# Kernel optimization log

Hardware: AMD Instinct MI355X
Metric: run time of the kernel (lower is better)

## Reference

```python
import jax, jax.numpy as jnp
import numpy as np

B, C, H, W = 128, 512, 14, 14
WIN, SHIFT = 7, 3
HEADS, HD = 16, 32
HID = 2048
EPS = 1e-5
N = WIN * WIN
NWH = H // WIN
NW = NWH * NWH


def _rel_pos_index():
    coords = np.stack(np.meshgrid(np.arange(WIN), np.arange(WIN), indexing='ij'))  # (2,Wh,Ww)
    flat = coords.reshape(2, -1)
    rel = (flat[:, :, None] - flat[:, None, :]).transpose(1, 2, 0)  # (N,N,2)
    rel[..., 0] += WIN - 1
    rel[..., 1] += WIN - 1
    rel[..., 0] *= 2 * WIN - 1
    return rel.sum(-1)  # (N,N) in [0, (2W-1)^2)


def _attn_mask():
    img = np.zeros((H, W))
    cnt = 0
    for h in (slice(0, -WIN), slice(-WIN, -SHIFT), slice(-SHIFT, None)):
        for w in (slice(0, -WIN), slice(-WIN, -SHIFT), slice(-SHIFT, None)):
            img[h, w] = cnt
            cnt += 1
    mw = img.reshape(NWH, WIN, NWH, WIN).transpose(0, 2, 1, 3).reshape(-1, N)  # (nW,N)
    d = mw[:, None, :] - mw[:, :, None]
    return np.where(d != 0, -100.0, 0.0).astype(np.float32)  # (nW,N,N)


REL_IDX = _rel_pos_index()
ATTN_MASK = jnp.asarray(_attn_mask())


def _ln_c(x, w, b):
    # LayerNorm2d: normalize over channel dim of NCHW
    mu = x.mean(axis=1, keepdims=True)
    var = ((x - mu) ** 2).mean(axis=1, keepdims=True)
    xn = (x - mu) * jax.lax.rsqrt(var + EPS)
    return xn * w[None, :, None, None] + b[None, :, None, None]


def setup_inputs() -> dict:
    key = jax.random.key(0)
    ks = jax.random.split(key, 12)
    s = 0.02
    return {
        'x': jax.random.normal(ks[0], (B, C, H, W), jnp.float32),
        'ln1_w': jnp.ones((C,), jnp.float32),
        'ln1_b': jnp.zeros((C,), jnp.float32),
        'qkv_w': jax.random.normal(ks[1], (3 * C, C), jnp.float32) * s,
        'qkv_b': jnp.zeros((3 * C,), jnp.float32),
        'rel_bias': jax.random.normal(ks[2], ((2 * WIN - 1) ** 2, HEADS), jnp.float32) * s,
        'proj_w': jax.random.normal(ks[3], (C, C), jnp.float32) * s,
        'proj_b': jnp.zeros((C,), jnp.float32),
        'gamma1': jnp.full((C,), 1e-6, jnp.float32),
        'ln2_w': jnp.ones((C,), jnp.float32),
        'ln2_b': jnp.zeros((C,), jnp.float32),
        'fc1_w': jax.random.normal(ks[4], (HID, C), jnp.float32) * s,
        'fc1_b': jnp.zeros((HID,), jnp.float32),
        'fc2_w': jax.random.normal(ks[5], (C, HID), jnp.float32) * s,
        'fc2_b': jnp.zeros((C,), jnp.float32),
        'gamma2': jnp.full((C,), 1e-6, jnp.float32),
    }


def reference(x, ln1_w, ln1_b, qkv_w, qkv_b, rel_bias, proj_w, proj_b, gamma1,
              ln2_w, ln2_b, fc1_w, fc1_b, fc2_w, fc2_b, gamma2):
    # ---- shifted-window attention branch ----
    y = _ln_c(x, ln1_w, ln1_b).transpose(0, 2, 3, 1)  # (B,H,W,C)
    y = jnp.roll(y, (-SHIFT, -SHIFT), axis=(1, 2))
    # window partition -> (B*nW, N, C)
    xw = y.reshape(B, NWH, WIN, NWH, WIN, C).transpose(0, 1, 3, 2, 4, 5).reshape(B * NW, N, C)
    qkv = (xw @ qkv_w.T + qkv_b).reshape(B * NW, N, 3, HEADS, HD).transpose(2, 0, 3, 1, 4)
    q, k, v = qkv[0], qkv[1], qkv[2]  # (B*nW, heads, N, hd)
    attn = jnp.einsum('bhnd,bhmd->bhnm', q * (HD ** -0.5), k)
    bias = rel_bias[REL_IDX.reshape(-1)].reshape(N, N, HEADS).transpose(2, 0, 1)  # (heads,N,N)
    attn = attn + bias[None]
    attn = attn.reshape(B, NW, HEADS, N, N) + ATTN_MASK[None, :, None]
    attn = jax.nn.softmax(attn.reshape(B * NW, HEADS, N, N), axis=-1)
    out = jnp.einsum('bhnm,bhmd->bhnd', attn, v).transpose(0, 2, 1, 3).reshape(B * NW, N, C)
    out = out @ proj_w.T + proj_b
    # window reverse + roll back
    y = out.reshape(B, NWH, NWH, WIN, WIN, C).transpose(0, 1, 3, 2, 4, 5).reshape(B, H, W, C)
    y = jnp.roll(y, (SHIFT, SHIFT), axis=(1, 2))
    y = gamma1 * y  # layer scale over channel (last dim in NHWC)
    x = x + y.transpose(0, 3, 1, 2)
    # ---- MLP branch ----
    z = _ln_c(x, ln2_w, ln2_b).transpose(0, 2, 3, 1)  # (B,H,W,C)
    z = jax.nn.gelu(z @ fc1_w.T + fc1_b, approximate=False)
    z = z @ fc2_w.T + fc2_b
    z = gamma2 * z
    return x + z.transpose(0, 3, 1, 2)
```

## Files before the change

### kernel.cpp

```cpp
#include <hip/hip_runtime.h>
#include <cmath>
#include <cstdint>

typedef float floatx4 __attribute__((ext_vector_type(4)));
typedef float floatx16 __attribute__((ext_vector_type(16)));
typedef int   intx4   __attribute__((ext_vector_type(4)));
typedef int   intx8   __attribute__((ext_vector_type(8)));

#define EPS_ 1e-5f
#define QSCALE 0.17677669529663689f

__device__ __forceinline__ void gload16(const uint8_t* g, uint8_t* l) {
  __builtin_amdgcn_global_load_lds(
      (const __attribute__((address_space(1))) void*)g,
      (__attribute__((address_space(3))) void*)l, 16, 0, 0);
}

template<bool HI>
__device__ __forceinline__ int pk_fp8(float a, float b, int old) {
  return __builtin_amdgcn_cvt_pk_fp8_f32(a, b, old, HI);
}
__device__ __forceinline__ int pk_fp8x4(float v0, float v1, float v2, float v3) {
  int w = pk_fp8<false>(v0, v1, 0);
  return pk_fp8<true>(v2, v3, w);
}

__device__ __forceinline__ uint16_t f2bf(float f) {
  uint32_t u = __float_as_uint(f);
  return (uint16_t)((u + 0x7fffu + ((u >> 16) & 1u)) >> 16);
}
__device__ __forceinline__ float bf2f(uint16_t h) {
  return __uint_as_float(((uint32_t)h) << 16);
}

__device__ __forceinline__ float fast_gelu(float v) {
  const float t = __expf(-1.702f * v);
  return v * __builtin_amdgcn_rcpf(1.f + t);
}

__device__ __forceinline__ intx8 cat8(intx4 a, intx4 b) {
  return __builtin_shufflevector(a, b, 0, 1, 2, 3, 4, 5, 6, 7);
}
__device__ __forceinline__ floatx16 mfma_mx(intx8 a, intx8 b, floatx16 c) {
  return __builtin_amdgcn_mfma_scale_f32_32x32x64_f8f6f4(
      a, b, c, 0, 0, 0, 0x7F7F7F7F, 0, 0x7F7F7F7F);
}


template<int K>
__global__ void cvt_frag(const float* __restrict__ s, uint8_t* __restrict__ d, int n4) {
  const int i = blockIdx.x * 256 + threadIdx.x;
  if (i >= n4) return;
  const int kq = K >> 2;
  const int n = i / kq;
  const int k = (i - n * kq) << 2;
  const float4 v = ((const float4*)s)[i];
  const int panel = ((n >> 6) << 2) + (n & 3);
  const int lm = (n >> 2) & 15;
  const long addr = (long)panel * (16 * K) + ((k >> 3) << 7) + (lm << 3) + (k & 4);
  *(int*)(d + addr) = pk_fp8x4(v.x, v.y, v.z, v.w);
}

__global__ void cvt_frag_mx512(const float* __restrict__ s, uint8_t* __restrict__ d, int n4) {
  const int i = blockIdx.x * 256 + threadIdx.x;
  if (i >= n4) return;
  const int n = i >> 7;
  const int k = (i & 127) << 2;
  const float4 v = ((const float4*)s)[i];
  const long addr = (long)(n >> 6) * 32768 + (n & 1) * 16384 + ((k >> 6) << 11)
                  + (((k >> 4) & 1) << 10)
                  + ((((k >> 5) & 1) << 5) + ((n & 63) >> 1)) * 16 + (k & 15);
  *(int*)(d + addr) = pk_fp8x4(v.x, v.y, v.z, v.w);
}

__global__ __launch_bounds__(256)
void ln_stats_nchw(const float* __restrict__ x, float* __restrict__ mu, float* __restrict__ rs) {
  const int tl = threadIdx.x & 63;
  const int wv = threadIdx.x >> 6;
  const int t = blockIdx.x * 64 + tl;
  const int b = t / 196;
  const int p = t - b * 196;
  const float* xp = x + (long)b * 100352 + p;
  float s = 0.f, ss = 0.f;
  const int cbeg = wv * 128;
  for (int c = cbeg; c < cbeg + 128; ++c) {
    const float v = xp[(long)c * 196];
    s += v; ss += v * v;
  }
  __shared__ float sb[4][64], qb[4][64];
  sb[wv][tl] = s; qb[wv][tl] = ss;
  __syncthreads();
  if (wv == 0) {
    s  = sb[0][tl] + sb[1][tl] + sb[2][tl] + sb[3][tl];
    ss = qb[0][tl] + qb[1][tl] + qb[2][tl] + qb[3][tl];
    const float m = s * (1.f / 512.f);
    const float var = ss * (1.f / 512.f) - m * m;
    mu[t] = m;
    rs[t] = rsqrtf(var + EPS_);
  }
}

__global__ __launch_bounds__(256)
void ln1_apply(const float* __restrict__ x, const float* __restrict__ mu, const float* __restrict__ rs,
               const float* __restrict__ w, const float* __restrict__ bb, uint8_t* __restrict__ A) {
  __shared__ float tile[64][53];
  const int bid = blockIdx.x;
  const int ct = bid & 7;
  const int pt = (bid >> 3) & 3;
  const int b = bid >> 5;
  const int p0 = pt * 49, c0 = ct * 64;
  const long xbase = (long)b * 100352;
  for (int idx = threadIdx.x; idx < 3136; idx += 256) {
    const int cl = idx / 49;
    const int pl = idx - cl * 49;
    tile[cl][pl] = x[xbase + (long)(c0 + cl) * 196 + p0 + pl];
  }
  __syncthreads();
  const int tbase = b * 196 + p0;
  for (int idx = threadIdx.x; idx < 784; idx += 256) {
    const int pl = idx >> 4;
    const int cq = (idx & 15) << 2;
    const int t = tbase + pl;
    const int c = c0 + cq;
    const float m = mu[t], rr = rs[t];
    const float v0 = (tile[cq + 0][pl] - m) * rr * w[c + 0] + bb[c + 0];
    const float v1 = (tile[cq + 1][pl] - m) * rr * w[c + 1] + bb[c + 1];
    const float v2 = (tile[cq + 2][pl] - m) * rr * w[c + 2] + bb[c + 2];
    const float v3 = (tile[cq + 3][pl] - m) * rr * w[c + 3] + bb[c + 3];
    const long addr = (long)(t & ~15) * 512 + ((c >> 3) << 7) + ((t & 15) << 3) + (c & 4);
    *(int*)(A + addr) = pk_fp8x4(v0, v1, v2, v3);
  }
}

__global__ __launch_bounds__(256)
void ln2_panel(const uint16_t* __restrict__ Xb, const float* __restrict__ S1,
               const float* __restrict__ S2, const float* __restrict__ w,
               const float* __restrict__ bb, uint8_t* __restrict__ Z) {
  __shared__ float xs[16 * 516];
  const int p = blockIdx.x;
  const int t0 = p * 16;
  for (int idx = threadIdx.x; idx < 1024; idx += 256) {
    const int tl = idx >> 6;
    const int c8 = (idx & 63) << 3;
    const uint4 raw = *(const uint4*)(Xb + ((long)(t0 + tl) << 9) + c8);
    float* xr = xs + tl * 516 + c8;
    xr[0] = bf2f((uint16_t)(raw.x & 0xffff)); xr[1] = bf2f((uint16_t)(raw.x >> 16));
    xr[2] = bf2f((uint16_t)(raw.y & 0xffff)); xr[3] = bf2f((uint16_t)(raw.y >> 16));
    xr[4] = bf2f((uint16_t)(raw.z & 0xffff)); xr[5] = bf2f((uint16_t)(raw.z >> 16));
    xr[6] = bf2f((uint16_t)(raw.w & 0xffff)); xr[7] = bf2f((uint16_t)(raw.w >> 16));
  }
  __syncthreads();
  for (int e = threadIdx.x; e < 2048; e += 256) {
    const int tl = e >> 7;
    const int c  = (e & 127) << 2;
    const int t = t0 + tl;
    const float m = S1[t] * (1.f / 512.f);
    const float var = S2[t] * (1.f / 512.f) - m * m;
    const float r = rsqrtf(var + EPS_);
    const float* xr = xs + tl * 516 + c;
    const float v0 = (xr[0] - m) * r * w[c + 0] + bb[c + 0];
    const float v1 = (xr[1] - m) * r * w[c + 1] + bb[c + 1];
    const float v2 = (xr[2] - m) * r * w[c + 2] + bb[c + 2];
    const float v3 = (xr[3] - m) * r * w[c + 3] + bb[c + 3];
    const long addr = (long)(t >> 5) * 16384 + ((c >> 5) << 10) + ((t & 31) << 5) + (c & 31);
    *(int*)(Z + addr) = pk_fp8x4(v0, v1, v2, v3);
  }
}

template<int MI, int K, int EPI, int NG, int T>
__global__ __launch_bounds__(256, 4)
void gemm_bl(const uint8_t* __restrict__ A, const uint8_t* __restrict__ Bw,
             const float* __restrict__ bias, const float* __restrict__ res,
             const uint16_t* __restrict__ resb, const float* __restrict__ gamma,
             uint8_t* __restrict__ outb, float* __restrict__ outf,
             uint16_t* __restrict__ outh, float* __restrict__ S1, float* __restrict__ S2,
             const int N) {
  const int kx = blockIdx.x & 7;
  const int sx = blockIdx.x >> 3;
  const int t = (sx / NG) * 8 + kx;
  if (t >= T) return;
  const int g = sx - (sx / NG) * NG;
  __shared__ __align__(16) uint8_t Bs[(EPI == 3) ? 33280 : 32768];
  const int tid = threadIdx.x;
  const int wave = tid >> 6, lane = tid & 63;
  const int lm = lane & 15, lq = lane >> 4;
  const long m0 = (long)t * (MI * 64);
  const long n0 = (long)g << 6;
  const uint8_t* abase = A + (m0 + wave * MI * 16) * (long)K + (lane << 3);
  floatx4 acc[MI][4] = {};
  constexpr int NKS = K / 32;
  long aP0[MI], aP1[MI];
  #pragma unroll
  for (int i = 0; i < MI; ++i) {
    aP0[i] = *(const long*)(abase + (long)i * 16 * K);
    aP1[i] = *(const long*)(abase + (long)i * 16 * K + 512);
  }
  #pragma unroll
  for (int ph = 0; ph < K / 512; ++ph) {
    const uint8_t* bsrc = Bw + n0 * K + ph * 8192;
    #pragma unroll
    for (int j = 0; j < 4; ++j)
      #pragma unroll
      for (int c = 0; c < 2; ++c)
        gload16(bsrc + (long)j * 16 * K + c * 4096 + tid * 16,
                Bs + j * 8192 + c * 4096 + tid * 16);
    __syncthreads();
    #pragma unroll
    for (int ksl = 0; ksl < 16; ++ksl) {
      const int sg = ph * 16 + ksl;
      long aC[MI];
      #pragma unroll
      for (int i = 0; i < MI; ++i) aC[i] = (ksl & 1) ? aP1[i] : aP0[i];
      if (sg + 2 < NKS) {
        #pragma unroll
        for (int i = 0; i < MI; ++i) {
          const long v = *(const long*)(abase + (long)i * 16 * K + (long)(sg + 2) * 512);
          if (ksl & 1) aP1[i] = v; else aP0[i] = v;
        }
      }
      long bf[4];
      #pragma unroll
      for (int j = 0; j < 4; ++j)
        bf[j] = *(const long*)(Bs + j * 8192 + ksl * 512 + (lane << 3));
      __builtin_amdgcn_s_setprio(1);
      #pragma unroll
      for (int i = 0; i < MI; ++i)
        #pragma unroll
        for (int j = 0; j < 4; ++j)
          acc[i][j] = __builtin_amdgcn_mfma_f32_16x16x32_fp8_fp8(aC[i], bf[j], acc[i][j], 0, 0, 0);
      __builtin_amdgcn_s_setprio(0);
    }
    if (K / 512 > 1 && ph + 1 < K / 512) __syncthreads();
  }
  const int cb = (g << 6) + (lm << 2);
  const float4 b4 = *(const float4*)(bias + cb);
  float4 g4 = make_float4(0.f, 0.f, 0.f, 0.f);
  if (EPI == 1 || EPI == 3) g4 = *(const float4*)(gamma + cb);
  const float qs = (EPI == 0 && cb < 512) ? QSCALE : 1.f;
  if (EPI != 3) {
    #pragma unroll
    for (int i = 0; i < MI; ++i) {
      #pragma unroll
      for (int r = 0; r < 4; ++r) {
        const long rowg = m0 + wave * MI * 16 + i * 16 + lq * 4 + r;
        float v0 = acc[i][0][r] + b4.x;
        float v1 = acc[i][1][r] + b4.y;
        float v2 = acc[i][2][r] + b4.z;
        float v3 = acc[i][3][r] + b4.w;
        if (EPI == 0) {
          *(int*)(outb + rowg * (long)N + cb) = pk_fp8x4(v0 * qs, v1 * qs, v2 * qs, v3 * qs);
        } else {
          const unsigned rg = (unsigned)rowg;
          const unsigned bi = rg / 196u;
          const unsigned p = rg - bi * 196u;
          const float* xr = res + (long)bi * 100352 + p;
          const float o0 = xr[(long)(cb + 0) * 196] + g4.x * v0;
          const float o1 = xr[(long)(cb + 1) * 196] + g4.y * v1;
          const float o2 = xr[(long)(cb + 2) * 196] + g4.z * v2;
          const float o3 = xr[(long)(cb + 3) * 196] + g4.w * v3;
          ushort4 hv;
          hv.x = f2bf(o0); hv.y = f2bf(o1); hv.z = f2bf(o2); hv.w = f2bf(o3);
          *(ushort4*)(outh + rowg * 512 + cb) = hv;
          const float q0 = bf2f(hv.x), q1 = bf2f(hv.y), q2 = bf2f(hv.z), q3 = bf2f(hv.w);
          float s = q0 + q1 + q2 + q3;
          float ss = q0 * q0 + q1 * q1 + q2 * q2 + q3 * q3;
          s += __shfl_xor(s, 1);  ss += __shfl_xor(ss, 1);
          s += __shfl_xor(s, 2);  ss += __shfl_xor(ss, 2);
          s += __shfl_xor(s, 4);  ss += __shfl_xor(ss, 4);
          s += __shfl_xor(s, 8);  ss += __shfl_xor(ss, 8);
          if (lm == 0) {
            atomicAdd(S1 + rowg, s);
            atomicAdd(S2 + rowg, ss);
          }
        }
      }
    }
  } else {
    float* Tx = (float*)Bs;
    __syncthreads();
    #pragma unroll
    for (int i = 0; i < MI; ++i) {
      #pragma unroll
      for (int r = 0; r < 4; ++r) {
        const long rowg = m0 + wave * MI * 16 + i * 16 + lq * 4 + r;
        const int rl = (int)(rowg - m0);
        const ushort4 rb = *(const ushort4*)(resb + rowg * 512 + cb);
        Tx[(lm * 4 + 0) * 129 + rl] = bf2f(rb.x) + g4.x * (acc[i][0][r] + b4.x);
        Tx[(lm * 4 + 1) * 129 + rl] = bf2f(rb.y) + g4.y * (acc[i][1][r] + b4.y);
        Tx[(lm * 4 + 2) * 129 + rl] = bf2f(rb.z) + g4.z * (acc[i][2][r] + b4.z);
        Tx[(lm * 4 + 3) * 129 + rl] = bf2f(rb.w) + g4.w * (acc[i][3][r] + b4.w);
      }
    }
    __syncthreads();
    #pragma unroll
    for (int t2 = 0; t2 < 32; ++t2) {
      const int idx = t2 * 256 + tid;
      const int rl = idx & 127;
      const int ch = idx >> 7;
      const unsigned m = (unsigned)(m0 + rl);
      const unsigned bi = m / 196u;
      const unsigned p = m - bi * 196u;
      outf[(long)bi * 100352 + (long)(n0 + ch) * 196 + p] = Tx[ch * 129 + rl];
    }
  }
}

__global__ __launch_bounds__(256, 4)
void gemm_mx_fc1(const uint8_t* __restrict__ A, const uint8_t* __restrict__ Bw,
                 const float* __restrict__ bias, uint8_t* __restrict__ outb) {
  const int kx = blockIdx.x & 7;
  const int sx = blockIdx.x >> 3;
  const int t = (sx >> 5) * 8 + kx;
  if (t >= 98) return;
  const int g = sx & 31;
  __shared__ __align__(16) uint8_t Bs[32768];
  const int tid = threadIdx.x;
  const int wave = tid >> 6, lane = tid & 63;
  const long m0 = (long)t * 256;
  const int n0 = g << 6;
  const uint8_t* bsrc = Bw + (long)n0 * 512;
  #pragma unroll
  for (int c = 0; c < 8; ++c)
    gload16(bsrc + c * 4096 + tid * 16, Bs + c * 4096 + tid * 16);
  const uint8_t* ab0 = A + (m0 + wave * 64) * 512 + lane * 32;
  const uint8_t* ab1 = ab0 + 16384;
  floatx16 acc[2][2] = {};
  __syncthreads();
  #pragma unroll
  for (int s = 0; s < 8; ++s) {
    const intx8 a0 = cat8(*(const intx4*)(ab0 + s * 2048), *(const intx4*)(ab0 + s * 2048 + 16));
    const intx8 a1 = cat8(*(const intx4*)(ab1 + s * 2048), *(const intx4*)(ab1 + s * 2048 + 16));
    const intx8 b0 = cat8(*(const intx4*)(Bs + s * 2048 + lane * 16),
                          *(const intx4*)(Bs + s * 2048 + 1024 + lane * 16));
    const intx8 b1 = cat8(*(const intx4*)(Bs + 16384 + s * 2048 + lane * 16),
                          *(const intx4*)(Bs + 16384 + s * 2048 + 1024 + lane * 16));
    acc[0][0] = mfma_mx(a0, b0, acc[0][0]);
    acc[0][1] = mfma_mx(a0, b1, acc[0][1]);
    acc[1][0] = mfma_mx(a1, b0, acc[1][0]);
    acc[1][1] = mfma_mx(a1, b1, acc[1][1]);
  }
  __syncthreads();
  uint8_t* Ex = Bs;
  const int cp = lane & 31;
  const int hl = cp << 1;
  const float2 b2 = *(const float2*)(bias + n0 + hl);
  const int hoff = ((hl >> 3) << 4) + (hl & 7);
  #pragma unroll
  for (int ri = 0; ri < 2; ++ri)
    #pragma unroll
    for (int q = 0; q < 16; ++q) {
      const int ml = wave * 64 + ri * 32 + 4 * (lane >> 5) + (q & 3) + 8 * (q >> 2);
      const float v0 = fast_gelu(acc[ri][0][q] + b2.x);
      const float v1 = fast_gelu(acc[ri][1][q] + b2.y);
      const int w = pk_fp8<false>(v0, v1, 0);
      const int laddr = ((ml >> 4) << 10) + (((ml & 15) >> 1) << 7) + ((ml & 1) << 3) + hoff;
      *(uint16_t*)(Ex + laddr) = (uint16_t)(w & 0xffff);
    }
  __syncthreads();
  #pragma unroll
  for (int t2 = 0; t2 < 4; ++t2) {
    const int u = t2 * 256 + tid;
    const long gaddr = (m0 + ((u >> 6) << 4)) * 2048 + (((long)(n0 >> 3) + (u & 7)) << 7)
                     + (((u >> 3) & 7) << 4);
    *(int4*)(outb + gaddr) = *(const int4*)(Ex + u * 16);
  }
}

__global__ __launch_bounds__(256)
void bm_build(const float* __restrict__ rel_bias, float* __restrict__ BM) {
  const int hw = blockIdx.x;
  const int head = hw >> 2, wpos = hw & 3;
  const int wi = wpos >> 1, wj = wpos & 1;
  for (int k = 0; k < 4; ++k) {
    const int idx = k * 256 + threadIdx.x;
    const int tile = idx >> 6, l = idx & 63;
    const int qi = tile >> 2, ti = tile & 3;
    const int n = l & 15, g = l >> 4;
    const int query = qi * 16 + n;
    const int qy = query / 7, qx = query - qy * 7;
    const int hh = wi * 7 + qy, ww = wj * 7 + qx;
    const int ri = (hh < 7 ? 0 : (hh < 11 ? 1 : 2)) * 3 + (ww < 7 ? 0 : (ww < 11 ? 1 : 2));
    float4 ov;
    float vv[4];
    #pragma unroll
    for (int r = 0; r < 4; ++r) {
      const int key = ti * 16 + g * 4 + r;
      float v;
      if (query >= 49 || key >= 49) {
        v = -3.0e38f;
      } else {
        const int ky = key / 7, kx = key - ky * 7;
        const int bidx = (qy - ky + 6) * 13 + (qx - kx + 6);
        const int h2 = wi * 7 + ky, w2 = wj * 7 + kx;
        const int rj = (h2 < 7 ? 0 : (h2 < 11 ? 1 : 2)) * 3 + (w2 < 7 ? 0 : (w2 < 11 ? 1 : 2));
        v = rel_bias[bidx * 16 + head] + ((ri != rj) ? -100.f : 0.f);
      }
      vv[r] = v;
    }
    ov.x = vv[0]; ov.y = vv[1]; ov.z = vv[2]; ov.w = vv[3];
    *(float4*)(BM + ((long)(hw * 16 + tile) << 8) + l * 4) = ov;
  }
}

__device__ __forceinline__ void tr4(const uint32_t d[4], uint32_t o[4]) {
  #pragma unroll
  for (int c = 0; c < 4; ++c)
    o[c] = ((d[0] >> (8 * c)) & 0xffu) | (((d[1] >> (8 * c)) & 0xffu) << 8)
         | (((d[2] >> (8 * c)) & 0xffu) << 16) | (((d[3] >> (8 * c)) & 0xffu) << 24);
}

__global__ __launch_bounds__(256)
void attn_mfma(const uint8_t* __restrict__ QKV, const float* __restrict__ BM,
               uint8_t* __restrict__ AT) {
  __shared__ uint8_t lds[4][9984];
  const int wave = threadIdx.x >> 6, lane = threadIdx.x & 63;
  const int n = lane & 15, g = lane >> 4;
  const int gw = blockIdx.x * 4 + wave;
  const int wd = gw >> 4, head = gw & 15;
  const int b = wd >> 2, wpos = wd & 3;
  const int wi = wpos >> 1, wj = wpos & 1;
  uint8_t* Pb = lds[wave];
  uint8_t* Vt = lds[wave] + 4608;
  uint8_t* Ot = lds[wave] + 6912;
  const long base = (long)b * 196 * 1536;
  auto tok = [&](int slot) -> int {
    const int ty = slot / 7, tx = slot - ty * 7;
    int h = wi * 7 + ty + 3; if (h >= 14) h -= 14;
    int w = wj * 7 + tx + 3; if (w >= 14) w -= 14;
    return h * 14 + w;
  };
  long Ak[4], Bq[4];
  #pragma unroll
  for (int t4 = 0; t4 < 4; ++t4) {
    int slot = t4 * 16 + n; if (slot > 48) slot = 48;
    const long tb = base + (long)tok(slot) * 1536 + head * 32 + g * 8;
    Bq[t4] = *(const long*)(QKV + tb);
    Ak[t4] = *(const long*)(QKV + tb + 512);
  }
  #pragma unroll
  for (int bb2 = 0; bb2 < 2; ++bb2) {
    const int blk = lane + bb2 * 64;
    const int dq = blk >> 4, tq = blk & 15;
    uint32_t d4[4], o4[4];
    #pragma unroll
    for (int r = 0; r < 4; ++r) {
      int slot = tq * 4 + r; if (slot > 48) slot = 48;
      d4[r] = *(const uint32_t*)(QKV + base + (long)tok(slot) * 1536 + 1024 + head * 32 + dq * 4);
    }
    tr4(d4, o4);
    #pragma unroll
    for (int c = 0; c < 4; ++c)
      *(uint32_t*)(Vt + (dq * 4 + c) * 72 + tq * 4) = o4[c];
  }
  floatx4 acc[4][4];
  const float* bmw = BM + ((long)(head * 4 + wpos) << 12) + lane * 4;
  #pragma unroll
  for (int qi = 0; qi < 4; ++qi)
    #pragma unroll
    for (int ti = 0; ti < 4; ++ti) {
      const float4 bv = *(const float4*)(bmw + ((qi * 4 + ti) << 8));
      acc[qi][ti][0] = bv.x; acc[qi][ti][1] = bv.y;
      acc[qi][ti][2] = bv.z; acc[qi][ti][3] = bv.w;
    }
  #pragma unroll
  for (int qi = 0; qi < 4; ++qi)
    #pragma unroll
    for (int ti = 0; ti < 4; ++ti)
      acc[qi][ti] = __builtin_amdgcn_mfma_f32_16x16x32_fp8_fp8(Ak[ti], Bq[qi], acc[qi][ti], 0, 0, 0);
  #pragma unroll
  for (int qi = 0; qi < 4; ++qi) {
    float mx = -3.0e38f;
    #pragma unroll
    for (int ti = 0; ti < 4; ++ti)
      #pragma unroll
      for (int r = 0; r < 4; ++r) mx = fmaxf(mx, acc[qi][ti][r]);
    mx = fmaxf(mx, __shfl_xor(mx, 16));
    mx = fmaxf(mx, __shfl_xor(mx, 32));
    float sum = 0.f;
    #pragma unroll
    for (int ti = 0; ti < 4; ++ti)
      #pragma unroll
      for (int r = 0; r < 4; ++r) {
        const float e = __expf(acc[qi][ti][r] - mx);
        acc[qi][ti][r] = e; sum += e;
      }
    sum += __shfl_xor(sum, 16);
    sum += __shfl_xor(sum, 32);
    const float inv = 1.f / sum;
    #pragma unroll
    for (int ti = 0; ti < 4; ++ti) {
      const int pw = pk_fp8x4(acc[qi][ti][0] * inv, acc[qi][ti][1] * inv,
                              acc[qi][ti][2] * inv, acc[qi][ti][3] * inv);
      *(uint32_t*)(Pb + (qi * 16 + n) * 72 + ti * 16 + g * 4) = pw;
    }
  }
  asm volatile("s_waitcnt lgkmcnt(0)" ::: "memory");
  long Bv[2][2];
  #pragma unroll
  for (int ni = 0; ni < 2; ++ni)
    #pragma unroll
    for (int s = 0; s < 2; ++s)
      Bv[ni][s] = *(const long*)(Vt + (ni * 16 + n) * 72 + s * 32 + g * 8);
  floatx4 o[4][2] = {};
  #pragma unroll
  for (int qi = 0; qi < 4; ++qi)
    #pragma unroll
    for (int s = 0; s < 2; ++s) {
      const long Ap = *(const long*)(Pb + (qi * 16 + n) * 72 + s * 32 + g * 8);
      #pragma unroll
      for (int ni = 0; ni < 2; ++ni)
        o[qi][ni] = __builtin_amdgcn_mfma_f32_16x16x32_fp8_fp8(Ap, Bv[ni][s], o[qi][ni], 0, 0, 0);
    }
  #pragma unroll
  for (int qi = 0; qi < 4; ++qi)
    #pragma unroll
    for (int ni = 0; ni < 2; ++ni)
      #pragma unroll
      for (int r = 0; r < 4; ++r)
        Ot[(qi * 16 + g * 4 + r) * 48 + ni * 16 + n] =
            (uint8_t)(pk_fp8<false>(o[qi][ni][r], 0.f, 0) & 0xff);
  asm volatile("s_waitcnt lgkmcnt(0)" ::: "memory");
  if (lane < 49) {
    const int m = b * 196 + tok(lane);
    uint8_t* opb = AT + (long)(m & ~15) * 512 + ((m & 15) << 3);
    #pragma unroll
    for (int d8 = 0; d8 < 4; ++d8)
      *(long*)(opb + (head * 4 + d8) * 128) = *(const long*)(Ot + lane * 48 + d8 * 8);
  }
}

extern "C" void kernel_launch(void* const* d_in, const int* in_sizes, int n_in,
                              void* d_out, int out_size, void* d_ws, size_t ws_size,
                              hipStream_t stream) {
  const float* x      = (const float*)d_in[0];
  const float* ln1_w  = (const float*)d_in[1];
  const float* ln1_b  = (const float*)d_in[2];
  const float* qkv_w  = (const float*)d_in[3];
  const float* qkv_b  = (const float*)d_in[4];
  const float* relb   = (const float*)d_in[5];
  const float* proj_w = (const float*)d_in[6];
  const float* proj_b = (const float*)d_in[7];
  const float* gamma1 = (const float*)d_in[8];
  const float* ln2_w  = (const float*)d_in[9];
  const float* ln2_b  = (const float*)d_in[10];
  const float* fc1_w  = (const float*)d_in[11];
  const float* fc1_b  = (const float*)d_in[12];
  const float* fc2_w  = (const float*)d_in[13];
  const float* fc2_b  = (const float*)d_in[14];
  const float* gamma2 = (const float*)d_in[15];
  float* out = (float*)d_out;
  char* ws = (char*)d_ws;

  float*    mu1 = (float*)(ws + 0);
  float*    rs1 = (float*)(ws + 100352);
  float*    S1  = (float*)(ws + 200704);
  float*    S2  = (float*)(ws + 301056);
  uint8_t*  Wq  = (uint8_t*)(ws + 401408);
  uint8_t*  Wp  = (uint8_t*)(ws + 1187840);
  uint8_t*  W1  = (uint8_t*)(ws + 1449984);
  uint8_t*  W2  = (uint8_t*)(ws + 2498560);
  float*    BMt = (float*)  (ws + 3547136);
  uint8_t*  Afp = (uint8_t*)(ws + 4595712);
  uint16_t* X1b = (uint16_t*)(ws + 68820992);
  uint8_t*  QKV = (uint8_t*)(ws + 120201216);
  uint8_t*  AT  = (uint8_t*)(ws + 158736384);
  uint8_t*  Hb  = (uint8_t*)(ws + 120201216);

  hipMemsetAsync(ws + 200704, 0, 200704, stream);

  cvt_frag<512> <<<768,  256, 0, stream>>>(qkv_w, Wq, 196608);
  cvt_frag<512> <<<256,  256, 0, stream>>>(proj_w, Wp, 65536);
  cvt_frag_mx512<<<1024, 256, 0, stream>>>(fc1_w, W1, 262144);
  cvt_frag<2048><<<1024, 256, 0, stream>>>(fc2_w, W2, 262144);
  bm_build<<<64, 256, 0, stream>>>(relb, BMt);

  ln_stats_nchw<<<392, 256, 0, stream>>>(x, mu1, rs1);
  ln1_apply<<<4096, 256, 0, stream>>>(x, mu1, rs1, ln1_w, ln1_b, Afp);

  gemm_bl<4, 512, 0, 24, 98><<<2496, 256, 0, stream>>>(Afp, Wq, qkv_b, nullptr, nullptr, nullptr, QKV, nullptr, nullptr, nullptr, nullptr, 1536);

  attn_mfma<<<2048, 256, 0, stream>>>(QKV, BMt, AT);

  gemm_bl<4, 512, 1, 8, 98><<<832, 256, 0, stream>>>(AT, Wp, proj_b, x, nullptr, gamma1, nullptr, nullptr, X1b, S1, S2, 512);

  ln2_panel<<<1568, 256, 0, stream>>>(X1b, S1, S2, ln2_w, ln2_b, Afp);

  gemm_mx_fc1<<<3328, 256, 0, stream>>>(Afp, W1, fc1_b, Hb);

  gemm_bl<2, 2048, 3, 8, 196><<<1600, 256, 0, stream>>>(Hb, W2, fc2_b, nullptr, X1b, gamma2, nullptr, out, nullptr, nullptr, nullptr, 512);
}
```

Baseline: 372.6 us.

## Move fc2 GEMM to MX fp8 32x32 MFMA kernel with matching hidden layout

Replaces the fc2 GEMM, which used the generic 16x16x32 fp8 kernel with 128-row tiles, with a dedicated kernel using the scaled 32x32 MX MFMA and 256x64 tiles, as already done for fc1. The fc1 epilogue now writes the hidden activation in the fragment layout this kernel expects, and fc2 weights are converted with a generalized MX fragment converter. The NCHW transpose epilogue runs in two halves through LDS to fit the larger tile. The aim is higher MFMA throughput and fewer, larger blocks. The cost is more output per block and a more serialized two-pass epilogue.

```diff
diff --git a/kernel.cpp b/kernel.cpp
--- a/kernel.cpp
+++ b/kernel.cpp
@@ -61,13 +61,15 @@
   *(int*)(d + addr) = pk_fp8x4(v.x, v.y, v.z, v.w);
 }
 
-__global__ void cvt_frag_mx512(const float* __restrict__ s, uint8_t* __restrict__ d, int n4) {
+template<int K>
+__global__ void cvt_frag_mx(const float* __restrict__ s, uint8_t* __restrict__ d, int n4) {
   const int i = blockIdx.x * 256 + threadIdx.x;
   if (i >= n4) return;
-  const int n = i >> 7;
-  const int k = (i & 127) << 2;
+  const int kq = K >> 2;
+  const int n = i / kq;
+  const int k = (i - n * kq) << 2;
   const float4 v = ((const float4*)s)[i];
-  const long addr = (long)(n >> 6) * 32768 + (n & 1) * 16384 + ((k >> 6) << 11)
+  const long addr = (long)(n >> 6) * (64 * K) + (long)(n & 1) * (32 * K) + ((k >> 6) << 11)
                   + (((k >> 4) & 1) << 10)
                   + ((((k >> 5) & 1) << 5) + ((n & 63) >> 1)) * 16 + (k & 15);
   *(int*)(d + addr) = pk_fp8x4(v.x, v.y, v.z, v.w);
@@ -171,8 +173,8 @@
 __global__ __launch_bounds__(256, 4)
 void gemm_bl(const uint8_t* __restrict__ A, const uint8_t* __restrict__ Bw,
              const float* __restrict__ bias, const float* __restrict__ res,
-             const uint16_t* __restrict__ resb, const float* __restrict__ gamma,
-             uint8_t* __restrict__ outb, float* __restrict__ outf,
+             const float* __restrict__ gamma,
+             uint8_t* __restrict__ outb,
              uint16_t* __restrict__ outh, float* __restrict__ S1, float* __restrict__ S2,
              const int N) {
   const int kx = blockIdx.x & 7;
@@ -180,7 +182,7 @@
   const int t = (sx / NG) * 8 + kx;
   if (t >= T) return;
   const int g = sx - (sx / NG) * NG;
-  __shared__ __align__(16) uint8_t Bs[(EPI == 3) ? 33280 : 32768];
+  __shared__ __align__(16) uint8_t Bs[32768];
   const int tid = threadIdx.x;
   const int wave = tid >> 6, lane = tid & 63;
   const int lm = lane & 15, lq = lane >> 4;
@@ -235,72 +237,43 @@
   const int cb = (g << 6) + (lm << 2);
   const float4 b4 = *(const float4*)(bias + cb);
   float4 g4 = make_float4(0.f, 0.f, 0.f, 0.f);
-  if (EPI == 1 || EPI == 3) g4 = *(const float4*)(gamma + cb);
+  if (EPI == 1) g4 = *(const float4*)(gamma + cb);
   const float qs = (EPI == 0 && cb < 512) ? QSCALE : 1.f;
-  if (EPI != 3) {
-    #pragma unroll
-    for (int i = 0; i < MI; ++i) {
-      #pragma unroll
-      for (int r = 0; r < 4; ++r) {
-        const long rowg = m0 + wave * MI * 16 + i * 16 + lq * 4 + r;
-        float v0 = acc[i][0][r] + b4.x;
-        float v1 = acc[i][1][r] + b4.y;
-        float v2 = acc[i][2][r] + b4.z;
-        float v3 = acc[i][3][r] + b4.w;
-        if (EPI == 0) {
-          *(int*)(outb + rowg * (long)N + cb) = pk_fp8x4(v0 * qs, v1 * qs, v2 * qs, v3 * qs);
-        } else {
-          const unsigned rg = (unsigned)rowg;
-          const unsigned bi = rg / 196u;
-          const unsigned p = rg - bi * 196u;
-          const float* xr = res + (long)bi * 100352 + p;
-          const float o0 = xr[(long)(cb + 0) * 196] + g4.x * v0;
-          const float o1 = xr[(long)(cb + 1) * 196] + g4.y * v1;
-          const float o2 = xr[(long)(cb + 2) * 196] + g4.z * v2;
-          const float o3 = xr[(long)(cb + 3) * 196] + g4.w * v3;
-          ushort4 hv;
-          hv.x = f2bf(o0); hv.y = f2bf(o1); hv.z = f2bf(o2); hv.w = f2bf(o3);
-          *(ushort4*)(outh + rowg * 512 + cb) = hv;
-          const float q0 = bf2f(hv.x), q1 = bf2f(hv.y), q2 = bf2f(hv.z), q3 = bf2f(hv.w);
-          float s = q0 + q1 + q2 + q3;
-          float ss = q0 * q0 + q1 * q1 + q2 * q2 + q3 * q3;
-          s += __shfl_xor(s, 1);  ss += __shfl_xor(ss, 1);
-          s += __shfl_xor(s, 2);  ss += __shfl_xor(ss, 2);
-          s += __shfl_xor(s, 4);  ss += __shfl_xor(ss, 4);
-          s += __shfl_xor(s, 8);  ss += __shfl_xor(ss, 8);
-          if (lm == 0) {
-            atomicAdd(S1 + rowg, s);
-            atomicAdd(S2 + rowg, ss);
-          }
+  #pragma unroll
+  for (int i = 0; i < MI; ++i) {
+    #pragma unroll
+    for (int r = 0; r < 4; ++r) {
+      const long rowg = m0 + wave * MI * 16 + i * 16 + lq * 4 + r;
+      float v0 = acc[i][0][r] + b4.x;
+      float v1 = acc[i][1][r] + b4.y;
+      float v2 = acc[i][2][r] + b4.z;
+      float v3 = acc[i][3][r] + b4.w;
+      if (EPI == 0) {
+        *(int*)(outb + rowg * (long)N + cb) = pk_fp8x4(v0 * qs, v1 * qs, v2 * qs, v3 * qs);
+      } else {
+        const unsigned rg = (unsigned)rowg;
+        const unsigned bi = rg / 196u;
+        const unsigned p = rg - bi * 196u;
+        const float* xr = res + (long)bi * 100352 + p;
+        const float o0 = xr[(long)(cb + 0) * 196] + g4.x * v0;
+        const float o1 = xr[(long)(cb + 1) * 196] + g4.y * v1;
+        const float o2 = xr[(long)(cb + 2) * 196] + g4.z * v2;
+        const float o3 = xr[(long)(cb + 3) * 196] + g4.w * v3;
+        ushort4 hv;
+        hv.x = f2bf(o0); hv.y = f2bf(o1); hv.z = f2bf(o2); hv.w = f2bf(o3);
+        *(ushort4*)(outh + rowg * 512 + cb) = hv;
+        const float q0 = bf2f(hv.x), q1 = bf2f(hv.y), q2 = bf2f(hv.z), q3 = bf2f(hv.w);
+        float s = q0 + q1 + q2 + q3;
+        float ss = q0 * q0 + q1 * q1 + q2 * q2 + q3 * q3;
+        s += __shfl_xor(s, 1);  ss += __shfl_xor(ss, 1);
+        s += __shfl_xor(s, 2);  ss += __shfl_xor(ss, 2);
+        s += __shfl_xor(s, 4);  ss += __shfl_xor(ss, 4);
+        s += __shfl_xor(s, 8);  ss += __shfl_xor(ss, 8);
+        if (lm == 0) {
+          atomicAdd(S1 + rowg, s);
+          atomicAdd(S2 + rowg, ss);
         }
       }
-    }
-  } else {
-    float* Tx = (float*)Bs;
-    __syncthreads();
-    #pragma unroll
-    for (int i = 0; i < MI; ++i) {
-      #pragma unroll
-      for (int r = 0; r < 4; ++r) {
-        const long rowg = m0 + wave * MI * 16 + i * 16 + lq * 4 + r;
-        const int rl = (int)(rowg - m0);
-        const ushort4 rb = *(const ushort4*)(resb + rowg * 512 + cb);
-        Tx[(lm * 4 + 0) * 129 + rl] = bf2f(rb.x) + g4.x * (acc[i][0][r] + b4.x);
-        Tx[(lm * 4 + 1) * 129 + rl] = bf2f(rb.y) + g4.y * (acc[i][1][r] + b4.y);
-        Tx[(lm * 4 + 2) * 129 + rl] = bf2f(rb.z) + g4.z * (acc[i][2][r] + b4.z);
-        Tx[(lm * 4 + 3) * 129 + rl] = bf2f(rb.w) + g4.w * (acc[i][3][r] + b4.w);
-      }
-    }
-    __syncthreads();
-    #pragma unroll
-    for (int t2 = 0; t2 < 32; ++t2) {
-      const int idx = t2 * 256 + tid;
-      const int rl = idx & 127;
-      const int ch = idx >> 7;
-      const unsigned m = (unsigned)(m0 + rl);
-      const unsigned bi = m / 196u;
-      const unsigned p = m - bi * 196u;
-      outf[(long)bi * 100352 + (long)(n0 + ch) * 196 + p] = Tx[ch * 129 + rl];
     }
   }
 }
@@ -344,7 +317,6 @@
   const int cp = lane & 31;
   const int hl = cp << 1;
   const float2 b2 = *(const float2*)(bias + n0 + hl);
-  const int hoff = ((hl >> 3) << 4) + (hl & 7);
   #pragma unroll
   for (int ri = 0; ri < 2; ++ri)
     #pragma unroll
@@ -353,16 +325,95 @@
       const float v0 = fast_gelu(acc[ri][0][q] + b2.x);
       const float v1 = fast_gelu(acc[ri][1][q] + b2.y);
       const int w = pk_fp8<false>(v0, v1, 0);
-      const int laddr = ((ml >> 4) << 10) + (((ml & 15) >> 1) << 7) + ((ml & 1) << 3) + hoff;
+      const int laddr = ((ml >> 5) << 11) + ((hl >> 5) << 10) + ((ml & 31) << 5) + (hl & 31);
       *(uint16_t*)(Ex + laddr) = (uint16_t)(w & 0xffff);
     }
   __syncthreads();
   #pragma unroll
   for (int t2 = 0; t2 < 4; ++t2) {
-    const int u = t2 * 256 + tid;
-    const long gaddr = (m0 + ((u >> 6) << 4)) * 2048 + (((long)(n0 >> 3) + (u & 7)) << 7)
-                     + (((u >> 3) & 7) << 4);
-    *(int4*)(outb + gaddr) = *(const int4*)(Ex + u * 16);
+    const int u16 = (t2 * 256 + tid) << 4;
+    const long gaddr = (long)(8 * t + (u16 >> 11)) * 65536
+                     + (((g << 1) + ((u16 >> 10) & 1)) << 10) + (u16 & 1023);
+    *(int4*)(outb + gaddr) = *(const int4*)(Ex + u16);
+  }
+}
+
+__global__ __launch_bounds__(256, 4)
+void gemm_mx_fc2(const uint8_t* __restrict__ A, const uint8_t* __restrict__ Bw,
+                 const float* __restrict__ bias, const uint16_t* __restrict__ resb,
+                 const float* __restrict__ gamma, float* __restrict__ outf) {
+  const int kx = blockIdx.x & 7;
+  const int sx = blockIdx.x >> 3;
+  const int t = (sx >> 3) * 8 + kx;
+  if (t >= 98) return;
+  const int g = sx & 7;
+  __shared__ __align__(16) uint8_t Bs[33280];
+  const int tid = threadIdx.x;
+  const int wave = tid >> 6, lane = tid & 63;
+  const long m0 = (long)t * 256;
+  const int n0 = g << 6;
+  const uint8_t* ab0 = A + (m0 + wave * 64) * 2048 + lane * 32;
+  const uint8_t* ab1 = ab0 + 65536;
+  const uint8_t* bbase = Bw + (long)g * 131072;
+  floatx16 acc[2][2] = {};
+  #pragma unroll
+  for (int ph = 0; ph < 4; ++ph) {
+    const uint8_t* be = bbase + ph * 16384;
+    #pragma unroll
+    for (int c = 0; c < 4; ++c) {
+      gload16(be + c * 4096 + tid * 16, Bs + c * 4096 + tid * 16);
+      gload16(be + 65536 + c * 4096 + tid * 16, Bs + 16384 + c * 4096 + tid * 16);
+    }
+    __syncthreads();
+    #pragma unroll
+    for (int s = 0; s < 8; ++s) {
+      const long ao = (long)(ph * 8 + s) * 2048;
+      const intx8 a0 = cat8(*(const intx4*)(ab0 + ao), *(const intx4*)(ab0 + ao + 16));
+      const intx8 a1 = cat8(*(const intx4*)(ab1 + ao), *(const intx4*)(ab1 + ao + 16));
+      const intx8 b0 = cat8(*(const intx4*)(Bs + s * 2048 + lane * 16),
+                            *(const intx4*)(Bs + s * 2048 + 1024 + lane * 16));
+      const intx8 b1 = cat8(*(const intx4*)(Bs + 16384 + s * 2048 + lane * 16),
+                            *(const intx4*)(Bs + 16384 + s * 2048 + 1024 + lane * 16));
+      acc[0][0] = mfma_mx(a0, b0, acc[0][0]);
+      acc[0][1] = mfma_mx(a0, b1, acc[0][1]);
+      acc[1][0] = mfma_mx(a1, b0, acc[1][0]);
+      acc[1][1] = mfma_mx(a1, b1, acc[1][1]);
+    }
+    __syncthreads();
+  }
+  float* Tx = (float*)Bs;
+  const int cp = lane & 31;
+  const int hl = cp << 1;
+  const float2 b2 = *(const float2*)(bias + n0 + hl);
+  const float2 g2 = *(const float2*)(gamma + n0 + hl);
+  #pragma unroll
+  for (int h = 0; h < 2; ++h) {
+    if ((wave >> 1) == h) {
+      #pragma unroll
+      for (int ri = 0; ri < 2; ++ri)
+        #pragma unroll
+        for (int q = 0; q < 16; ++q) {
+          const int ml = wave * 64 + ri * 32 + 4 * (lane >> 5) + (q & 3) + 8 * (q >> 2);
+          const int rl = ml & 127;
+          const uint32_t xr = *(const uint32_t*)(resb + (m0 + ml) * 512 + n0 + hl);
+          const float o0 = bf2f((uint16_t)(xr & 0xffff)) + g2.x * (acc[ri][0][q] + b2.x);
+          const float o1 = bf2f((uint16_t)(xr >> 16))    + g2.y * (acc[ri][1][q] + b2.y);
+          Tx[hl * 129 + rl] = o0;
+          Tx[(hl + 1) * 129 + rl] = o1;
+        }
+    }
+    __syncthreads();
+    #pragma unroll
+    for (int t2 = 0; t2 < 32; ++t2) {
+      const int idx = t2 * 256 + tid;
+      const int rl = idx & 127;
+      const int ch = idx >> 7;
+      const unsigned m = (unsigned)(m0 + h * 128 + rl);
+      const unsigned bi = m / 196u;
+      const unsigned p = m - bi * 196u;
+      outf[(long)bi * 100352 + (long)(n0 + ch) * 196 + p] = Tx[ch * 129 + rl];
+    }
+    if (h == 0) __syncthreads();
   }
 }
 
@@ -570,22 +621,22 @@
 
   cvt_frag<512> <<<768,  256, 0, stream>>>(qkv_w, Wq, 196608);
   cvt_frag<512> <<<256,  256, 0, stream>>>(proj_w, Wp, 65536);
-  cvt_frag_mx512<<<1024, 256, 0, stream>>>(fc1_w, W1, 262144);
-  cvt_frag<2048><<<1024, 256, 0, stream>>>(fc2_w, W2, 262144);
+  cvt_frag_mx<512> <<<1024, 256, 0, stream>>>(fc1_w, W1, 262144);
+  cvt_frag_mx<2048><<<1024, 256, 0, stream>>>(fc2_w, W2, 262144);
   bm_build<<<64, 256, 0, stream>>>(relb, BMt);
 
   ln_stats_nchw<<<392, 256, 0, stream>>>(x, mu1, rs1);
   ln1_apply<<<4096, 256, 0, stream>>>(x, mu1, rs1, ln1_w, ln1_b, Afp);
 
-  gemm_bl<4, 512, 0, 24, 98><<<2496, 256, 0, stream>>>(Afp, Wq, qkv_b, nullptr, nullptr, nullptr, QKV, nullptr, nullptr, nullptr, nullptr, 1536);
+  gemm_bl<4, 512, 0, 24, 98><<<2496, 256, 0, stream>>>(Afp, Wq, qkv_b, nullptr, nullptr, QKV, nullptr, nullptr, nullptr, 1536);
 
   attn_mfma<<<2048, 256, 0, stream>>>(QKV, BMt, AT);
 
-  gemm_bl<4, 512, 1, 8, 98><<<832, 256, 0, stream>>>(AT, Wp, proj_b, x, nullptr, gamma1, nullptr, nullptr, X1b, S1, S2, 512);
+  gemm_bl<4, 512, 1, 8, 98><<<832, 256, 0, stream>>>(AT, Wp, proj_b, x, gamma1, nullptr, X1b, S1, S2, 512);
 
   ln2_panel<<<1568, 256, 0, stream>>>(X1b, S1, S2, ln2_w, ln2_b, Afp);
 
   gemm_mx_fc1<<<3328, 256, 0, stream>>>(Afp, W1, fc1_b, Hb);
 
-  gemm_bl<2, 2048, 3, 8, 196><<<1600, 256, 0, stream>>>(Hb, W2, fc2_b, nullptr, X1b, gamma2, nullptr, out, nullptr, nullptr, nullptr, 512);
-}
+  gemm_mx_fc2<<<832, 256, 0, stream>>>(Hb, W2, fc2_b, X1b, gamma2, out);
+}
```

New measurement: 548.0 us. +47.1%, slower.
